# Performance work log

Hardware: AMD Instinct MI355X
Metric: run time of the kernel (lower is better)

The kernel has to match this reference:

```python
import jax, jax.numpy as jnp
import numpy as np

NUM_NODES = 50000
D_IN = 256
D_OUT = 256
N_QUERIES = 128
PER_GROUP = 256            # edges per query group in the last step (> max_edges)
E1 = N_QUERIES * PER_GROUP # 32768
E0 = 32768
RATIO = 0.2                # ratio_update


def setup_inputs() -> dict:
    key = jax.random.key(0)
    ks = jax.random.split(key, 10)
    d4 = 4 * D_IN
    rng = np.random.default_rng(0)
    # last-step edges: col0 = query idx (sorted, equal-size groups), col6 = src, col7 = dst
    edges1 = np.zeros((E1, 8), np.int64)
    edges1[:, 0] = np.repeat(np.arange(N_QUERIES), PER_GROUP)
    edges1[:, 6] = rng.integers(0, NUM_NODES, E1)
    edges1[:, 7] = rng.integers(0, NUM_NODES, E1)
    # earlier-step edges
    edges0 = np.zeros((E0, 8), np.int64)
    edges0[:, 0] = rng.integers(0, N_QUERIES, E0)
    edges0[:, 6] = rng.integers(0, NUM_NODES, E0)
    edges0[:, 7] = rng.integers(0, NUM_NODES, E0)
    return {
        "visited_node_score": jax.random.uniform(ks[0], (NUM_NODES,), jnp.float32),
        "visited_node_representation": jax.random.normal(ks[1], (NUM_NODES, D_IN), jnp.float32),
        "selected_edges0": jnp.asarray(edges0),
        "selected_edges1": jnp.asarray(edges1),
        "rel_emb0": jax.random.normal(ks[2], (E0, D_IN), jnp.float32),
        "rel_emb1": jax.random.normal(ks[3], (E1, D_IN), jnp.float32),
        "query_src_ts_emb": jax.random.normal(ks[4], (N_QUERIES, D_IN), jnp.float32),
        "query_rel_emb": jax.random.normal(ks[5], (N_QUERIES, D_IN), jnp.float32),
        "Wq": jax.random.normal(ks[6], (d4, d4), jnp.float32) * np.sqrt(2.0 / d4),
        "Wk": jax.random.normal(ks[7], (d4, d4), jnp.float32) * np.sqrt(2.0 / d4),
        "Wl": jax.random.normal(ks[8], (D_OUT, D_IN), jnp.float32) * np.sqrt(2.0 / (D_IN + D_OUT)),
        "bl": jnp.zeros((D_OUT,), jnp.float32),
        "max_edges": 64,
    }


def _att_score(edges, node_repr, rel, qst_tab, qr_tab, Wq, Wk):
    # G3: sum(Q(cat(vi,rel,qst,qr)) * K(cat(vj,rel,qst,qr)), -1) per edge
    q, src, dst = edges[:, 0], edges[:, 6], edges[:, 7]
    qst, qr = qst_tab[q], qr_tab[q]
    left = jnp.concatenate([node_repr[src], rel, qst, qr], axis=-1)   # [E, 4d]
    right = jnp.concatenate([node_repr[dst], rel, qst, qr], axis=-1)  # [E, 4d]
    return jnp.sum((left @ Wq.T) * (right @ Wk.T), axis=-1)          # [E]


def _seg_softmax(logits, seg, n):
    m = jax.ops.segment_max(logits, seg, num_segments=n)
    e = jnp.exp(logits - m[seg])
    s = jax.ops.segment_sum(e, seg, num_segments=n)
    return e / s[seg]


def _update_repr(edges, node_repr, w, ratio):
    # sparse mm: out[src] += (1-ratio)*w_e*repr[dst]; + identity for non-src rows, + ratio*repr for src rows
    src, dst = edges[:, 6], edges[:, 7]
    n = node_repr.shape[0]
    agg = jax.ops.segment_sum(((1.0 - ratio) * w)[:, None] * node_repr[dst], src, num_segments=n)
    is_src = jnp.zeros((n,), bool).at[src].set(True)
    diag = jnp.where(is_src, ratio, 1.0)
    return agg + diag[:, None] * node_repr


def reference(visited_node_score, visited_node_representation, selected_edges0,
              selected_edges1, rel_emb0, rel_emb1, query_src_ts_emb, query_rel_emb,
              Wq, Wk, Wl, bl, max_edges):
    n = visited_node_representation.shape[0]
    nq = query_src_ts_emb.shape[0]
    pg = selected_edges1.shape[0] // nq
    # attention on last step's edges
    logits = _att_score(selected_edges1, visited_node_representation, rel_emb1,
                        query_src_ts_emb, query_rel_emb, Wq, Wk)
    src1 = selected_edges1[:, 6]
    src_score = visited_node_score[src1]
    soft = _seg_softmax(logits, src1, n)
    target = soft * src_score
    # per-query-group top-k pruning (each group has pg > k edges)
    _, ti = jax.lax.top_k(target.reshape(nq, pg), max_edges)  # [nq, k]
    orig_indices = (ti + (jnp.arange(nq) * pg)[:, None]).reshape(-1)
    pruned_edges = selected_edges1[orig_indices]
    pruned_src_score = src_score[orig_indices]
    pruned_soft = soft[orig_indices]
    # sparse scatter-aggregation of scores onto dst (col 7)
    updated_node_score = jax.ops.segment_sum(pruned_soft * pruned_src_score,
                                             pruned_edges[:, 7], num_segments=n)
    node_repr = _update_repr(pruned_edges, visited_node_representation, pruned_soft, RATIO)
    # back-propagate representations through the earlier step
    tl = _att_score(selected_edges0, node_repr, rel_emb0, query_src_ts_emb, query_rel_emb, Wq, Wk)
    ts = _seg_softmax(tl, selected_edges0[:, 6], n)
    node_repr = _update_repr(selected_edges0, node_repr, ts, RATIO)
    # bypass_forward: LeakyReLU(Linear(.))
    node_repr = jax.nn.leaky_relu(node_repr @ Wl.T + bl)
    return (updated_node_score, node_repr, pruned_edges, orig_indices)
```

## Files before the change

### kernel.cpp

```cpp
#include <hip/hip_runtime.h>

#define NN 50000
#define D 256
#define NQ 128
#define PG 256
#define NE 32768
#define ME 64
#define BCAP 32
#define KDIM 256
#define NKT 8

typedef _Float16 f16;
typedef __attribute__((ext_vector_type(4))) _Float16 f16x4;
typedef __attribute__((ext_vector_type(8))) _Float16 f16x8;
typedef __attribute__((ext_vector_type(4))) float f32x4;

#define MFMA16(a,b,c) __builtin_amdgcn_mfma_f32_16x16x32_f16(a,b,c,0,0,0)

__device__ __forceinline__ unsigned fenc(float f){
  unsigned b = __float_as_uint(f);
  return (b & 0x80000000u) ? ~b : (b | 0x80000000u);
}
__device__ __forceinline__ float fdec(unsigned u){
  unsigned b = (u & 0x80000000u) ? (u & 0x7fffffffu) : ~u;
  return __uint_as_float(b);
}
__device__ __forceinline__ void split8(float4 a, float4 b, f16x8& h, f16x8& l){
  float v[8] = {a.x,a.y,a.z,a.w,b.x,b.y,b.z,b.w};
#pragma unroll
  for (int i=0;i<8;++i){
    _Float16 hh = (_Float16)v[i];
    h[i] = hh;
    l[i] = (_Float16)(v[i] - (float)hh);
  }
}

template<int EPI>
__global__ __launch_bounds__(256) void hgemm(const float* __restrict__ A,
                                             int Mrows,
                                             const f16* __restrict__ Bh, const f16* __restrict__ Bl,
                                             float* __restrict__ C, int ldc,
                                             const float* __restrict__ bias)
{
  __shared__ f16 AsH[128*40], AsL[128*40], BsH[128*40], BsL[128*40];
  const int tid = threadIdx.x;
  const int rb = blockIdx.x*128, cb = blockIdx.y*128;
  const int row = tid >> 1, ko = (tid & 1)*16;
  const bool aok = (rb + row) < Mrows;
  const int lane = tid & 63, wv = tid >> 6;
  const int qrw = (wv & 1)*64, qcw = (wv >> 1)*64;
  const int lm = lane & 15, qd = lane >> 4;

  const float* gA = A + (size_t)(rb+row)*KDIM + ko;
  const f16* gBh = Bh + (size_t)(cb+row)*KDIM + ko;
  const f16* gBl = Bl + (size_t)(cb+row)*KDIM + ko;

  float4 pa0=make_float4(0.f,0.f,0.f,0.f), pa1=pa0, pa2=pa0, pa3=pa0;
  f16x8 pbh0, pbh1, pbl0, pbl1;
  if (aok){ pa0 = *(const float4*)gA;     pa1 = *(const float4*)(gA+4);
            pa2 = *(const float4*)(gA+8); pa3 = *(const float4*)(gA+12); }
  pbh0 = *(const f16x8*)gBh; pbh1 = *(const f16x8*)(gBh+8);
  pbl0 = *(const f16x8*)gBl; pbl1 = *(const f16x8*)(gBl+8);

  f32x4 acc[4][4];
#pragma unroll
  for (int t=0;t<4;++t)
#pragma unroll
    for (int u=0;u<4;++u)
#pragma unroll
      for (int r=0;r<4;++r) acc[t][u][r] = 0.f;

  const int wbase = row*40 + ko;
  for (int kt = 0; kt < NKT; ++kt){
    __syncthreads();
    {
      f16x8 h0,h1,l0,l1;
      split8(pa0,pa1,h0,l0); split8(pa2,pa3,h1,l1);
      *(f16x8*)(AsH + wbase) = h0; *(f16x8*)(AsH + wbase + 8) = h1;
      *(f16x8*)(AsL + wbase) = l0; *(f16x8*)(AsL + wbase + 8) = l1;
      *(f16x8*)(BsH + wbase) = pbh0; *(f16x8*)(BsH + wbase + 8) = pbh1;
      *(f16x8*)(BsL + wbase) = pbl0; *(f16x8*)(BsL + wbase + 8) = pbl1;
    }
    __syncthreads();
    if (kt+1 < NKT){
      const int k0 = (kt+1)*32;
      if (aok){ pa0 = *(const float4*)(gA + k0);     pa1 = *(const float4*)(gA + k0 + 4);
                pa2 = *(const float4*)(gA + k0 + 8); pa3 = *(const float4*)(gA + k0 + 12); }
      pbh0 = *(const f16x8*)(gBh + k0); pbh1 = *(const f16x8*)(gBh + k0 + 8);
      pbl0 = *(const f16x8*)(gBl + k0); pbl1 = *(const f16x8*)(gBl + k0 + 8);
    }
    f16x8 fah[4], fal[4], fbh[4], fbl[4];
#pragma unroll
    for (int t=0;t<4;++t){
      int off = (qrw + t*16 + lm)*40 + qd*8;
      fah[t] = *(const f16x8*)(AsH + off);
      fal[t] = *(const f16x8*)(AsL + off);
    }
#pragma unroll
    for (int u=0;u<4;++u){
      int off = (qcw + u*16 + lm)*40 + qd*8;
      fbh[u] = *(const f16x8*)(BsH + off);
      fbl[u] = *(const f16x8*)(BsL + off);
    }
#pragma unroll
    for (int t=0;t<4;++t)
#pragma unroll
      for (int u=0;u<4;++u){
        acc[t][u] = MFMA16(fah[t], fbh[u], acc[t][u]);
        acc[t][u] = MFMA16(fah[t], fbl[u], acc[t][u]);
        acc[t][u] = MFMA16(fal[t], fbh[u], acc[t][u]);
      }
  }
#pragma unroll
  for (int t=0;t<4;++t){
#pragma unroll
    for (int u=0;u<4;++u){
      int col = cb + qcw + u*16 + lm;
      f32x4 v = acc[t][u];
#pragma unroll
      for (int r=0;r<4;++r){
        int rg = rb + qrw + t*16 + qd*4 + r;
        if (rg < Mrows){
          float x = v[r];
          if (EPI==1){ x += bias[col]; x = x > 0.f ? x : 0.01f*x; }
          C[(size_t)rg*ldc + col] = x;
        }
      }
    }
  }
}

__global__ __launch_bounds__(256) void hgemm_rel(const float* __restrict__ A,
                                                 const f16* __restrict__ Bh, const f16* __restrict__ Bl,
                                                 const int* __restrict__ edges,
                                                 const float* __restrict__ H,
                                                 const float* __restrict__ Rel,
                                                 float* __restrict__ logits)
{
  __shared__ f16 AsH[128*40], AsL[128*40], BsH[128*40], BsL[128*40];
  __shared__ int sIdx[128];
  const int tid = threadIdx.x;
  const int rb = blockIdx.x*128, cb = blockIdx.y*128;
  const int sec = blockIdx.y >> 1;
  const int row = tid >> 1, ko = (tid & 1)*16;
  const int lane = tid & 63, wv = tid >> 6;
  const int qrw = (wv & 1)*64, qcw = (wv >> 1)*64;
  const int lm = lane & 15, qd = lane >> 4;

  if (tid < 128){
    int e = rb + tid;
    sIdx[tid] = (sec==0) ? edges[(size_t)e*8+6] : (sec==1 ? edges[(size_t)e*8+7] : 0);
  }

  const float* gA = A + (size_t)(rb+row)*KDIM + ko;
  const f16* gBh = Bh + (size_t)(cb+row)*KDIM + ko;
  const f16* gBl = Bl + (size_t)(cb+row)*KDIM + ko;

  float4 pa0 = *(const float4*)gA,     pa1 = *(const float4*)(gA+4);
  float4 pa2 = *(const float4*)(gA+8), pa3 = *(const float4*)(gA+12);
  f16x8 pbh0 = *(const f16x8*)gBh, pbh1 = *(const f16x8*)(gBh+8);
  f16x8 pbl0 = *(const f16x8*)gBl, pbl1 = *(const f16x8*)(gBl+8);

  f32x4 acc[4][4];
#pragma unroll
  for (int t=0;t<4;++t)
#pragma unroll
    for (int u=0;u<4;++u)
#pragma unroll
      for (int r=0;r<4;++r) acc[t][u][r] = 0.f;

  const int wbase = row*40 + ko;
  for (int kt = 0; kt < NKT; ++kt){
    __syncthreads();
    {
      f16x8 h0,h1,l0,l1;
      split8(pa0,pa1,h0,l0); split8(pa2,pa3,h1,l1);
      *(f16x8*)(AsH + wbase) = h0; *(f16x8*)(AsH + wbase + 8) = h1;
      *(f16x8*)(AsL + wbase) = l0; *(f16x8*)(AsL + wbase + 8) = l1;
      *(f16x8*)(BsH + wbase) = pbh0; *(f16x8*)(BsH + wbase + 8) = pbh1;
      *(f16x8*)(BsL + wbase) = pbl0; *(f16x8*)(BsL + wbase + 8) = pbl1;
    }
    __syncthreads();
    if (kt+1 < NKT){
      const int k0 = (kt+1)*32;
      pa0 = *(const float4*)(gA + k0);     pa1 = *(const float4*)(gA + k0 + 4);
      pa2 = *(const float4*)(gA + k0 + 8); pa3 = *(const float4*)(gA + k0 + 12);
      pbh0 = *(const f16x8*)(gBh + k0); pbh1 = *(const f16x8*)(gBh + k0 + 8);
      pbl0 = *(const f16x8*)(gBl + k0); pbl1 = *(const f16x8*)(gBl + k0 + 8);
    }
    f16x8 fah[4], fal[4], fbh[4], fbl[4];
#pragma unroll
    for (int t=0;t<4;++t){
      int off = (qrw + t*16 + lm)*40 + qd*8;
      fah[t] = *(const f16x8*)(AsH + off);
      fal[t] = *(const f16x8*)(AsL + off);
    }
#pragma unroll
    for (int u=0;u<4;++u){
      int off = (qcw + u*16 + lm)*40 + qd*8;
      fbh[u] = *(const f16x8*)(BsH + off);
      fbl[u] = *(const f16x8*)(BsL + off);
    }
#pragma unroll
    for (int t=0;t<4;++t)
#pragma unroll
      for (int u=0;u<4;++u){
        acc[t][u] = MFMA16(fah[t], fbh[u], acc[t][u]);
        acc[t][u] = MFMA16(fah[t], fbl[u], acc[t][u]);
        acc[t][u] = MFMA16(fal[t], fbh[u], acc[t][u]);
      }
  }
  const int cbase = ((blockIdx.y & 1)*128) + qcw + lm;
#pragma unroll
  for (int t=0;t<4;++t){
#pragma unroll
    for (int r=0;r<4;++r){
      int lrow = qrw + t*16 + qd*4 + r;
      int e = rb + lrow;
      const float* xb = (sec==2) ? (Rel + (size_t)e*256)
                                 : (H + (size_t)sIdx[lrow]*256);
      float p = acc[t][0][r]*xb[cbase]
              + acc[t][1][r]*xb[cbase+16]
              + acc[t][2][r]*xb[cbase+32]
              + acc[t][3][r]*xb[cbase+48];
      p += __shfl_xor(p, 1); p += __shfl_xor(p, 2);
      p += __shfl_xor(p, 4); p += __shfl_xor(p, 8);
      if (lm == 0) atomicAdd(logits + e, p);
    }
  }
}

__global__ void split_f16(const float* __restrict__ X, f16* __restrict__ Xh,
                          f16* __restrict__ Xl, int n)
{
  int i = (blockIdx.x*256 + threadIdx.x)*4;
  if (i >= n) return;
  float4 v = *(const float4*)(X+i);
  f16x4 h, l;
  h[0]=(_Float16)v.x; h[1]=(_Float16)v.y; h[2]=(_Float16)v.z; h[3]=(_Float16)v.w;
  l[0]=(_Float16)(v.x-(float)h[0]); l[1]=(_Float16)(v.y-(float)h[1]);
  l[2]=(_Float16)(v.z-(float)h[2]); l[3]=(_Float16)(v.w-(float)h[3]);
  *(f16x4*)(Xh+i)=h; *(f16x4*)(Xl+i)=l;
}

__global__ void build_bt_mhh(const float* __restrict__ M, f16* __restrict__ Bh, f16* __restrict__ Bl)
{
  int idx = blockIdx.x*256 + threadIdx.x;
  int n = idx >> 8, k = idx & 255;
  float v = M[(size_t)k*1024 + n];
  _Float16 h = (_Float16)v;
  Bh[idx] = h; Bl[idx] = (_Float16)(v - (float)h);
}

__global__ void build_bt_wcat(const float* __restrict__ M, f16* __restrict__ Bh, f16* __restrict__ Bl)
{
  int idx = blockIdx.x*256 + threadIdx.x;
  int j = idx >> 8, k = idx & 255;
  float v;
  if (j < 256)      v = M[(size_t)j*1024 + 256 + k];
  else if (j < 512) v = M[(size_t)(256+k)*1024 + (j-256)];
  else              v = M[(size_t)(256 + j-512)*1024 + 256 + k];
  _Float16 h = (_Float16)v;
  Bh[idx] = h; Bl[idx] = (_Float16)(v - (float)h);
}

__global__ __launch_bounds__(256) void gemm_tn_split(const float* __restrict__ A,
                                                     const float* __restrict__ B,
                                                     double* __restrict__ Cpart)
{
  __shared__ double As[16][66];
  __shared__ double Bs[16][66];
  const int tid = threadIdx.x;
  const int rb = blockIdx.x * 64, cb = blockIdx.y * 64;
  const int z  = blockIdx.z;
  const int ty = tid >> 4, tx = tid & 15;
  const int aj = tid >> 4, akk = (tid & 15) << 2;
  double acc[4][4] = {};
  const int jbeg = z * 128;
  float4 av = *(const float4*)(A + (size_t)(jbeg+aj)*1024 + rb + akk);
  float4 bv = *(const float4*)(B + (size_t)(jbeg+aj)*1024 + cb + akk);
  for (int t0 = 0; t0 < 8; ++t0) {
    __syncthreads();
    As[aj][akk+0]=(double)av.x; As[aj][akk+1]=(double)av.y;
    As[aj][akk+2]=(double)av.z; As[aj][akk+3]=(double)av.w;
    Bs[aj][akk+0]=(double)bv.x; Bs[aj][akk+1]=(double)bv.y;
    Bs[aj][akk+2]=(double)bv.z; Bs[aj][akk+3]=(double)bv.w;
    __syncthreads();
    if (t0 < 7){
      int j0 = jbeg + (t0+1)*16;
      av = *(const float4*)(A + (size_t)(j0+aj)*1024 + rb + akk);
      bv = *(const float4*)(B + (size_t)(j0+aj)*1024 + cb + akk);
    }
#pragma unroll
    for (int jj=0; jj<16; ++jj){
      double2 a01 = *(const double2*)&As[jj][ty*4];
      double2 a23 = *(const double2*)&As[jj][ty*4+2];
      double2 b01 = *(const double2*)&Bs[jj][tx*4];
      double2 b23 = *(const double2*)&Bs[jj][tx*4+2];
      double a0=a01.x, a1=a01.y, a2=a23.x, a3=a23.y;
      double b0=b01.x, b1=b01.y, b2=b23.x, b3=b23.y;
      acc[0][0]+=a0*b0; acc[0][1]+=a0*b1; acc[0][2]+=a0*b2; acc[0][3]+=a0*b3;
      acc[1][0]+=a1*b0; acc[1][1]+=a1*b1; acc[1][2]+=a1*b2; acc[1][3]+=a1*b3;
      acc[2][0]+=a2*b0; acc[2][1]+=a2*b1; acc[2][2]+=a2*b2; acc[2][3]+=a2*b3;
      acc[3][0]+=a3*b0; acc[3][1]+=a3*b1; acc[3][2]+=a3*b2; acc[3][3]+=a3*b3;
    }
  }
  double* Cz = Cpart + (size_t)z * 1048576;
#pragma unroll
  for (int i=0;i<4;++i)
#pragma unroll
    for (int j=0;j<4;++j)
      Cz[(size_t)(rb+ty*4+i)*1024 + cb+tx*4+j] = acc[i][j];
}

__global__ void reduce_m(const double* __restrict__ P, float* __restrict__ Mout)
{
  int i = blockIdx.x*256 + threadIdx.x;
  double s = 0.0;
#pragma unroll
  for (int z=0;z<8;++z) s += P[(size_t)i + (size_t)z*1048576];
  Mout[i] = (float)s;
}

__global__ void build_g(const float* __restrict__ qst, const float* __restrict__ qr,
                        float* __restrict__ G)
{
  int idx = blockIdx.x*256 + threadIdx.x;
  int q = idx >> 9, k = idx & 511;
  G[idx] = (k < 256) ? qst[(size_t)q*256 + k] : qr[(size_t)q*256 + k - 256];
}

__global__ void build_bq(const float* __restrict__ M, float* __restrict__ Bq)
{
  int idx = blockIdx.x*256 + threadIdx.x;
  int k = idx / 1280, t = idx - k*1280;
  float v;
  if (t < 256)      v = M[(size_t)t*1024 + 512 + k];
  else if (t < 512) v = M[(size_t)(512+k)*1024 + (t-256)];
  else if (t < 768) v = M[(size_t)(256+(t-512))*1024 + 512 + k]
                      + M[(size_t)(512+k)*1024 + 256 + (t-512)];
  else              v = M[(size_t)(512+k)*1024 + 512 + (t-768)];
  Bq[idx] = v;
}

__global__ __launch_bounds__(256) void gemm64(const float* __restrict__ A, int lda,
                                              const float* __restrict__ B, int ldb,
                                              float* __restrict__ C, int ldc,
                                              int Mrows, int Kdim)
{
  __shared__ float As[16][68];
  __shared__ float Bs[16][68];
  const int tid = threadIdx.x;
  const int rb = blockIdx.x*64, cb = blockIdx.y*64;
  const int tx = tid & 15, ty = tid >> 4;
  const int a_r = tid >> 2, a_k = (tid & 3)*4;
  const int b_c = tid & 63, b_r0 = (tid >> 6)*4;
  const bool aok = (rb + a_r) < Mrows;
  float4 pa = make_float4(0.f,0.f,0.f,0.f);
  float pb[4];
  if (aok) pa = *(const float4*)(A + (size_t)(rb+a_r)*lda + a_k);
#pragma unroll
  for (int j=0;j<4;++j) pb[j] = B[(size_t)(b_r0+j)*ldb + cb + b_c];
  float acc[4][4] = {};
  const int NK = Kdim >> 4;
  for (int t0=0; t0<NK; ++t0){
    __syncthreads();
    As[a_k+0][a_r]=pa.x; As[a_k+1][a_r]=pa.y; As[a_k+2][a_r]=pa.z; As[a_k+3][a_r]=pa.w;
#pragma unroll
    for (int j=0;j<4;++j) Bs[b_r0+j][b_c] = pb[j];
    __syncthreads();
    if (t0+1 < NK){
      int k0 = (t0+1) << 4;
      if (aok) pa = *(const float4*)(A + (size_t)(rb+a_r)*lda + k0 + a_k);
#pragma unroll
      for (int j=0;j<4;++j) pb[j] = B[(size_t)(k0+b_r0+j)*ldb + cb + b_c];
    }
#pragma unroll
    for (int kk=0;kk<16;++kk){
      float a[4], b[4];
      *(float4*)&a[0] = *(const float4*)&As[kk][ty*4];
#pragma unroll
      for (int j=0;j<4;++j) b[j] = Bs[kk][tx + 16*j];
#pragma unroll
      for (int i=0;i<4;++i)
#pragma unroll
        for (int j=0;j<4;++j) acc[i][j] += a[i]*b[j];
    }
  }
#pragma unroll
  for (int i=0;i<4;++i){
    int r = rb + ty*4 + i;
    if (r < Mrows)
#pragma unroll
      for (int j=0;j<4;++j)
        C[(size_t)r*ldc + cb + tx + 16*j] = acc[i][j];
  }
}

__global__ __launch_bounds__(256) void qc_dot(const float* __restrict__ Ccat,
    const float* __restrict__ qst, const float* __restrict__ qr, float* __restrict__ qc)
{
  __shared__ float red[256];
  int q = blockIdx.x, t = threadIdx.x;
  float a = Ccat[(size_t)q*1280 + 768 + t]  * qst[(size_t)q*256 + t]
          + Ccat[(size_t)q*1280 + 1024 + t] * qr [(size_t)q*256 + t];
  red[t] = a;
  __syncthreads();
  for (int s=128; s>0; s>>=1){
    if (t < s) red[t] += red[t+s];
    __syncthreads();
  }
  if (t==0) qc[q] = red[0];
}

__global__ __launch_bounds__(256) void slim_logits(const int* __restrict__ edges,
    const float* __restrict__ H, const float* __restrict__ U,
    const float* __restrict__ Rel,
    const float* __restrict__ Ct, const float* __restrict__ qc,
    float* __restrict__ logits)
{
  int lane = threadIdx.x & 63;
  int e = blockIdx.x*4 + (threadIdx.x >> 6);
  int q   = edges[(size_t)e*8 + 0];
  int src = edges[(size_t)e*8 + 6];
  int dst = edges[(size_t)e*8 + 7];
  const float4* hs = (const float4*)(H   + (size_t)src*256);
  const float4* hd = (const float4*)(H   + (size_t)dst*256);
  const float4* us = (const float4*)(U   + (size_t)src*256);
  const float4* rl = (const float4*)(Rel + (size_t)e*256);
  const float4* t1 = (const float4*)(Ct + (size_t)q*1280);
  const float4* t2 = (const float4*)(Ct + (size_t)q*1280 + 256);
  const float4* w4 = (const float4*)(Ct + (size_t)q*1280 + 512);
  float4 a, b, c;
  float s = 0.f;
  a = hd[lane]; b = us[lane]; c = t2[lane];
  s += a.x*(b.x+c.x) + a.y*(b.y+c.y) + a.z*(b.z+c.z) + a.w*(b.w+c.w);
  a = hs[lane]; c = t1[lane];
  s += a.x*c.x + a.y*c.y + a.z*c.z + a.w*c.w;
  a = rl[lane]; c = w4[lane];
  s += a.x*c.x + a.y*c.y + a.z*c.z + a.w*c.w;
#pragma unroll
  for (int off=32; off>0; off>>=1) s += __shfl_down(s, off);
  if (lane==0) logits[e] = s + qc[q];
}

__global__ void segmax_k(const int* __restrict__ edges, const float* __restrict__ logits,
                         unsigned* __restrict__ menc, int nE)
{
  int e = blockIdx.x*256 + threadIdx.x; if (e >= nE) return;
  atomicMax(menc + edges[(size_t)e*8+6], fenc(logits[e]));
}
__global__ void segexp_k(const int* __restrict__ edges, const float* __restrict__ logits,
                         const unsigned* __restrict__ menc, float* __restrict__ ebuf,
                         float* __restrict__ ssum, int nE)
{
  int e = blockIdx.x*256 + threadIdx.x; if (e >= nE) return;
  int s = edges[(size_t)e*8+6];
  float ex = expf(logits[e] - fdec(menc[s]));
  ebuf[e] = ex;
  atomicAdd(ssum + s, ex);
}
template<int TGT>
__global__ void segsoft_k(const int* __restrict__ edges, const float* __restrict__ ebuf,
                          const float* __restrict__ ssum, float* __restrict__ soft,
                          const float* __restrict__ score, float* __restrict__ target, int nE)
{
  int e = blockIdx.x*256 + threadIdx.x; if (e >= nE) return;
  int s = edges[(size_t)e*8+6];
  float so = ebuf[e] / ssum[s];
  soft[e] = so;
  if (TGT) target[e] = so * score[s];
}

__global__ __launch_bounds__(256) void topk_k(const float* __restrict__ target,
    const float* __restrict__ soft, const int* __restrict__ edges1,
    float* __restrict__ out0, float* __restrict__ out2, float* __restrict__ out3,
    int* __restrict__ p_src, int* __restrict__ p_dst, float* __restrict__ p_w)
{
  int qb = blockIdx.x, t = threadIdx.x;
  __shared__ float v[256];
  __shared__ int   ix[256];
  v[t] = target[(size_t)qb*256 + t];
  ix[t] = t;
  __syncthreads();
  for (int k=2; k<=256; k<<=1){
    for (int j=k>>1; j>0; j>>=1){
      int ixj = t ^ j;
      if (ixj > t){
        float va=v[t], vb=v[ixj]; int ia=ix[t], ib=ix[ixj];
        bool dir  = ((t & k) == 0);
        bool l_ab = (va > vb) || (va == vb && ia < ib);
        bool sw   = dir ? (!l_ab) : l_ab;
        if (sw){ v[t]=vb; v[ixj]=va; ix[t]=ib; ix[ixj]=ia; }
      }
      __syncthreads();
    }
  }
  if (t < 64){
    int oi = qb*256 + ix[t];
    int o  = qb*64 + t;
    out3[o] = (float)oi;
#pragma unroll
    for (int c2=0;c2<8;++c2) out2[(size_t)o*8 + c2] = (float)edges1[(size_t)oi*8 + c2];
    int s_ = edges1[(size_t)oi*8+6], d_ = edges1[(size_t)oi*8+7];
    p_src[o] = s_; p_dst[o] = d_; p_w[o] = soft[oi];
    atomicAdd(out0 + d_, v[t]);
  }
}

__global__ void bucket_fill(const int* __restrict__ srcarr, int stride, int n,
                            int* __restrict__ counts, int* __restrict__ bucket,
                            int* __restrict__ over, int* __restrict__ n_over)
{
  int e = blockIdx.x*256 + threadIdx.x; if (e >= n) return;
  int s = srcarr[(size_t)e*stride];
  int pos = atomicAdd(counts + s, 1);
  if (pos < BCAP) bucket[(size_t)s*BCAP + pos] = e;
  else { int oi = atomicAdd(n_over, 1); over[oi] = e; }
}

__global__ __launch_bounds__(256) void fused_update(const int* __restrict__ counts,
    const int* __restrict__ bucket, const int* __restrict__ dstarr, int dstride,
    const float* __restrict__ w, const float* __restrict__ Hin, float* __restrict__ Hout)
{
  int lane = threadIdx.x & 63;
  int n = blockIdx.x*4 + (threadIdx.x >> 6);
  if (n >= NN) return;
  int cnt = counts[n];
  float fac = cnt > 0 ? 0.2f : 1.0f;
  float4 h = ((const float4*)(Hin + (size_t)n*256))[lane];
  float4 acc = make_float4(fac*h.x, fac*h.y, fac*h.z, fac*h.w);
  int m = cnt < BCAP ? cnt : BCAP;
  for (int i=0;i<m;++i){
    int e = bucket[(size_t)n*BCAP + i];
    int d = dstarr[(size_t)e*dstride];
    float f = 0.8f * w[e];
    float4 vv = ((const float4*)(Hin + (size_t)d*256))[lane];
    acc.x += f*vv.x; acc.y += f*vv.y; acc.z += f*vv.z; acc.w += f*vv.w;
  }
  ((float4*)(Hout + (size_t)n*256))[lane] = acc;
}

__global__ __launch_bounds__(256) void over_k(const int* __restrict__ over,
    const int* __restrict__ n_over,
    const int* __restrict__ srcarr, int sstride,
    const int* __restrict__ dstarr, int dstride,
    const float* __restrict__ w, const float* __restrict__ Hin, float* __restrict__ Hout)
{
  int lane = threadIdx.x & 63;
  int i = blockIdx.x*4 + (threadIdx.x >> 6);
  if (i >= *n_over) return;
  int e = over[i];
  int s = srcarr[(size_t)e*sstride], d = dstarr[(size_t)e*dstride];
  float f = 0.8f * w[e];
  float4 vv = ((const float4*)(Hin + (size_t)d*256))[lane];
  float* o = Hout + (size_t)s*256 + lane*4;
  atomicAdd(o+0, f*vv.x); atomicAdd(o+1, f*vv.y);
  atomicAdd(o+2, f*vv.z); atomicAdd(o+3, f*vv.w);
}

extern "C" void kernel_launch(void* const* d_in, const int* in_sizes, int n_in,
                              void* d_out, int out_size, void* d_ws, size_t ws_size,
                              hipStream_t stream)
{
  const float* score = (const float*)d_in[0];
  const float* H0    = (const float*)d_in[1];
  const int*   edges0= (const int*)d_in[2];
  const int*   edges1= (const int*)d_in[3];
  const float* rel0  = (const float*)d_in[4];
  const float* rel1  = (const float*)d_in[5];
  const float* qst   = (const float*)d_in[6];
  const float* qr    = (const float*)d_in[7];
  const float* Wq    = (const float*)d_in[8];
  const float* Wk    = (const float*)d_in[9];
  const float* Wl    = (const float*)d_in[10];
  const float* bl    = (const float*)d_in[11];
  (void)in_sizes; (void)n_in; (void)out_size; (void)ws_size;

  float* out0 = (float*)d_out;
  float* out1 = out0 + NN;
  float* out2 = out1 + (size_t)NN*D;
  float* out3 = out2 + (size_t)NQ*ME*8;

  float* ws     = (float*)d_ws;
  float* Mbuf   = ws;
  float* Ccat   = ws + 1048576;
  float* qcv    = ws + 1212416;
  float* G      = ws + 1212544;
  float* logits = ws + 1278080;
  float* ebuf   = ws + 1310848;
  float* soft   = ws + 1343616;
  float* target = ws + 1376384;
  unsigned* menc= (unsigned*)(ws + 1409152);
  float* ssum   = ws + 1459152;
  int* p_src    = (int*)(ws + 1509152);
  int* p_dst    = (int*)(ws + 1517344);
  float* p_w    = ws + 1525536;
  float* Bq     = ws + 1533728;
  float* U      = ws + 2189088;
  float* Hnew   = ws + 14989088;
  float* SCR    = ws + 27789088;
  int* counts = (int*)SCR;
  int* n_over = (int*)(SCR + 50000);
  int* over   = (int*)(SCR + 50056);
  int* bucket = (int*)(SCR + 100000);
  float* P0   = SCR + 2000000;
  double* Mpart = (double*)P0;
  f16* mhh_h  = (f16*)P0;
  f16* mhh_l  = (f16*)(P0 + 32768);
  f16* wcat_h = (f16*)(P0 + 65536);
  f16* wcat_l = (f16*)(P0 + 163840);
  f16* wl_h   = (f16*)(P0 + 262144);
  f16* wl_l   = (f16*)(P0 + 294912);
  float* Hpre = U;

  hipMemsetAsync(out0, 0, (size_t)NN*4, stream);
  hipMemsetAsync(menc, 0, (size_t)NN*4, stream);
  hipMemsetAsync(ssum, 0, (size_t)NN*4, stream);

  gemm_tn_split<<<dim3(16,16,8), 256, 0, stream>>>(Wq, Wk, Mpart);
  reduce_m<<<4096, 256, 0, stream>>>(Mpart, Mbuf);
  build_g<<<256, 256, 0, stream>>>(qst, qr, G);
  build_bq<<<2560, 256, 0, stream>>>(Mbuf, Bq);
  gemm64<<<dim3(2,20), 256, 0, stream>>>(G, 512, Bq, 1280, Ccat, 1280, NQ, 512);
  qc_dot<<<NQ, 256, 0, stream>>>(Ccat, qst, qr, qcv);
  build_bt_mhh<<<256, 256, 0, stream>>>(Mbuf, mhh_h, mhh_l);
  build_bt_wcat<<<768, 256, 0, stream>>>(Mbuf, wcat_h, wcat_l);
  split_f16<<<64, 256, 0, stream>>>(Wl, wl_h, wl_l, 65536);

  hgemm<0><<<dim3(391,2), 256, 0, stream>>>(H0, NN, mhh_h, mhh_l, U, 256, nullptr);
  slim_logits<<<NE/4, 256, 0, stream>>>(edges1, H0, U, rel1, Ccat, qcv, logits);
  hgemm_rel<<<dim3(256,6), 256, 0, stream>>>(rel1, wcat_h, wcat_l, edges1, H0, rel1, logits);

  segmax_k<<<NE/256, 256, 0, stream>>>(edges1, logits, menc, NE);
  segexp_k<<<NE/256, 256, 0, stream>>>(edges1, logits, menc, ebuf, ssum, NE);
  segsoft_k<1><<<NE/256, 256, 0, stream>>>(edges1, ebuf, ssum, soft, score, target, NE);

  topk_k<<<NQ, 256, 0, stream>>>(target, soft, edges1, out0, out2, out3, p_src, p_dst, p_w);

  hipMemsetAsync(counts, 0, (size_t)NN*4, stream);
  hipMemsetAsync(n_over, 0, 4, stream);
  bucket_fill<<<(NQ*ME+255)/256, 256, 0, stream>>>(p_src, 1, NQ*ME, counts, bucket, over, n_over);
  fused_update<<<(NN+3)/4, 256, 0, stream>>>(counts, bucket, p_dst, 1, p_w, H0, Hnew);
  over_k<<<(NQ*ME)/4, 256, 0, stream>>>(over, n_over, p_src, 1, p_dst, 1, p_w, H0, Hnew);

  hipMemsetAsync(menc, 0, (size_t)NN*4, stream);
  hipMemsetAsync(ssum, 0, (size_t)NN*4, stream);

  hgemm<0><<<dim3(391,2), 256, 0, stream>>>(Hnew, NN, mhh_h, mhh_l, U, 256, nullptr);
  slim_logits<<<NE/4, 256, 0, stream>>>(edges0, Hnew, U, rel0, Ccat, qcv, logits);
  hgemm_rel<<<dim3(256,6), 256, 0, stream>>>(rel0, wcat_h, wcat_l, edges0, Hnew, rel0, logits);

  segmax_k<<<NE/256, 256, 0, stream>>>(edges0, logits, menc, NE);
  segexp_k<<<NE/256, 256, 0, stream>>>(edges0, logits, menc, ebuf, ssum, NE);
  segsoft_k<0><<<NE/256, 256, 0, stream>>>(edges0, ebuf, ssum, soft, nullptr, nullptr, NE);

  hipMemsetAsync(counts, 0, (size_t)NN*4, stream);
  hipMemsetAsync(n_over, 0, 4, stream);
  bucket_fill<<<NE/256, 256, 0, stream>>>(edges0 + 6, 8, NE, counts, bucket, over, n_over);
  fused_update<<<(NN+3)/4, 256, 0, stream>>>(counts, bucket, edges0 + 7, 8, soft, Hnew, Hpre);
  over_k<<<NE/4, 256, 0, stream>>>(over, n_over, edges0 + 6, 8, edges0 + 7, 8, soft, Hnew, Hpre);

  hgemm<1><<<dim3(391,2), 256, 0, stream>>>(Hpre, NN, wl_h, wl_l, out1, 256, bl);
}
```

Measured before the change: 618.8 us.

## Replace split-K fp64 Wq^T Wk GEMM plus reduction with single full-K kernel

After: 650.0 us. 5.0% more time.

```diff
diff --git a/kernel.cpp b/kernel.cpp
--- a/kernel.cpp
+++ b/kernel.cpp
@@ -264,39 +264,52 @@
   Bh[idx] = h; Bl[idx] = (_Float16)(v - (float)h);
 }
 
-__global__ __launch_bounds__(256) void gemm_tn_split(const float* __restrict__ A,
-                                                     const float* __restrict__ B,
-                                                     double* __restrict__ Cpart)
-{
-  __shared__ double As[16][66];
-  __shared__ double Bs[16][66];
+__global__ __launch_bounds__(256) void gemm_tn_full(const float* __restrict__ A,
+                                                    const float* __restrict__ B,
+                                                    float* __restrict__ Mout)
+{
+  __shared__ __align__(16) double As[16*82];
+  __shared__ __align__(16) double Bs[16*82];
   const int tid = threadIdx.x;
   const int rb = blockIdx.x * 64, cb = blockIdx.y * 64;
-  const int z  = blockIdx.z;
   const int ty = tid >> 4, tx = tid & 15;
-  const int aj = tid >> 4, akk = (tid & 15) << 2;
+  const int aj = tid >> 4, ag = tid & 15;
   double acc[4][4] = {};
-  const int jbeg = z * 128;
-  float4 av = *(const float4*)(A + (size_t)(jbeg+aj)*1024 + rb + akk);
-  float4 bv = *(const float4*)(B + (size_t)(jbeg+aj)*1024 + cb + akk);
-  for (int t0 = 0; t0 < 8; ++t0) {
-    __syncthreads();
-    As[aj][akk+0]=(double)av.x; As[aj][akk+1]=(double)av.y;
-    As[aj][akk+2]=(double)av.z; As[aj][akk+3]=(double)av.w;
-    Bs[aj][akk+0]=(double)bv.x; Bs[aj][akk+1]=(double)bv.y;
-    Bs[aj][akk+2]=(double)bv.z; Bs[aj][akk+3]=(double)bv.w;
-    __syncthreads();
-    if (t0 < 7){
-      int j0 = jbeg + (t0+1)*16;
-      av = *(const float4*)(A + (size_t)(j0+aj)*1024 + rb + akk);
-      bv = *(const float4*)(B + (size_t)(j0+aj)*1024 + cb + akk);
+  double tot[4][4] = {};
+
+  const float* gA = A + (size_t)aj*1024 + rb + ag*4;
+  const float* gB = B + (size_t)aj*1024 + cb + ag*4;
+  float4 av = *(const float4*)gA;
+  float4 bv = *(const float4*)gB;
+
+  const int wbase = aj*82 + (ag>>1)*10 + (ag&1)*4;
+  const int aoff  = (ty>>1)*10 + (ty&1)*4;
+  const int boff  = (tx>>1)*10 + (tx&1)*4;
+
+  for (int slab = 0; slab < 64; ++slab) {
+    __syncthreads();
+    {
+      double2* wa = (double2*)(As + wbase);
+      double2* wb = (double2*)(Bs + wbase);
+      wa[0] = make_double2((double)av.x, (double)av.y);
+      wa[1] = make_double2((double)av.z, (double)av.w);
+      wb[0] = make_double2((double)bv.x, (double)bv.y);
+      wb[1] = make_double2((double)bv.z, (double)bv.w);
+    }
+    __syncthreads();
+    if (slab < 63){
+      gA += 16*1024; gB += 16*1024;
+      av = *(const float4*)gA;
+      bv = *(const float4*)gB;
     }
 #pragma unroll
     for (int jj=0; jj<16; ++jj){
-      double2 a01 = *(const double2*)&As[jj][ty*4];
-      double2 a23 = *(const double2*)&As[jj][ty*4+2];
-      double2 b01 = *(const double2*)&Bs[jj][tx*4];
-      double2 b23 = *(const double2*)&Bs[jj][tx*4+2];
+      const double* pa = As + jj*82 + aoff;
+      const double* pb = Bs + jj*82 + boff;
+      double2 a01 = *(const double2*)(pa);
+      double2 a23 = *(const double2*)(pa+2);
+      double2 b01 = *(const double2*)(pb);
+      double2 b23 = *(const double2*)(pb+2);
       double a0=a01.x, a1=a01.y, a2=a23.x, a3=a23.y;
       double b0=b01.x, b1=b01.y, b2=b23.x, b3=b23.y;
       acc[0][0]+=a0*b0; acc[0][1]+=a0*b1; acc[0][2]+=a0*b2; acc[0][3]+=a0*b3;
@@ -304,22 +317,18 @@
       acc[2][0]+=a2*b0; acc[2][1]+=a2*b1; acc[2][2]+=a2*b2; acc[2][3]+=a2*b3;
       acc[3][0]+=a3*b0; acc[3][1]+=a3*b1; acc[3][2]+=a3*b2; acc[3][3]+=a3*b3;
     }
-  }
-  double* Cz = Cpart + (size_t)z * 1048576;
+    if ((slab & 7) == 7){
+#pragma unroll
+      for (int i=0;i<4;++i)
+#pragma unroll
+        for (int j=0;j<4;++j){ tot[i][j] += acc[i][j]; acc[i][j] = 0.0; }
+    }
+  }
 #pragma unroll
   for (int i=0;i<4;++i)
 #pragma unroll
     for (int j=0;j<4;++j)
-      Cz[(size_t)(rb+ty*4+i)*1024 + cb+tx*4+j] = acc[i][j];
-}
-
-__global__ void reduce_m(const double* __restrict__ P, float* __restrict__ Mout)
-{
-  int i = blockIdx.x*256 + threadIdx.x;
-  double s = 0.0;
-#pragma unroll
-  for (int z=0;z<8;++z) s += P[(size_t)i + (size_t)z*1048576];
-  Mout[i] = (float)s;
+      Mout[(size_t)(rb+ty*4+i)*1024 + cb+tx*4+j] = (float)tot[i][j];
 }
 
 __global__ void build_g(const float* __restrict__ qst, const float* __restrict__ qr,
@@ -605,7 +614,6 @@
   int* over   = (int*)(SCR + 50056);
   int* bucket = (int*)(SCR + 100000);
   float* P0   = SCR + 2000000;
-  double* Mpart = (double*)P0;
   f16* mhh_h  = (f16*)P0;
   f16* mhh_l  = (f16*)(P0 + 32768);
   f16* wcat_h = (f16*)(P0 + 65536);
@@ -618,8 +626,7 @@
   hipMemsetAsync(menc, 0, (size_t)NN*4, stream);
   hipMemsetAsync(ssum, 0, (size_t)NN*4, stream);
 
-  gemm_tn_split<<<dim3(16,16,8), 256, 0, stream>>>(Wq, Wk, Mpart);
-  reduce_m<<<4096, 256, 0, stream>>>(Mpart, Mbuf);
+  gemm_tn_full<<<dim3(16,16), 256, 0, stream>>>(Wq, Wk, Mbuf);
   build_g<<<256, 256, 0, stream>>>(qst, qr, G);
   build_bq<<<2560, 256, 0, stream>>>(Mbuf, Bq);
   gemm64<<<dim3(2,20), 256, 0, stream>>>(G, 512, Bq, 1280, Ccat, 1280, NQ, 512);
```
